# Performance work log

Measured on AMD Instinct MI355X. Metric: run time of the kernel, lower is better.

## Reference

```python
import jax, jax.numpy as jnp
import numpy as np

B, H, N, D, T = 4, 16, 1024, 64, 4

def setup_inputs() -> dict:
    key = jax.random.key(0)
    kq, kk, kv, ka, kw = jax.random.split(key, 5)
    Q = jax.random.normal(kq, (B, H, N, D), dtype=jnp.float32)
    K = jax.random.normal(kk, (B, H, N, D), dtype=jnp.float32)
    V = jax.random.normal(kv, (B, H, N, D), dtype=jnp.float32)
    # stacked adjacency matrices, one [B, N, N] per edge type
    A = jax.random.uniform(ka, (T, B, N, N), dtype=jnp.float32)
    # per-edge-type, per-head learned scalar bias weights (glorot-init scalars in torch)
    weight_E = jax.random.normal(kw, (T, H), dtype=jnp.float32)
    return {"Q": Q, "K": K, "V": V, "A": A, "weight_E": weight_E}

def reference(Q, K, V, A, weight_E):
    scale = Q.shape[-1] ** 0.5
    # raw scores [B, H, N, N]
    attn_score = jnp.einsum("bhnd,bhmd->bhnm", Q, K)
    # B_E = sum_t attn_score * (A_t * w_t)  ->  attn_score * sum_t (A_t * w_t)
    bias_factor = jnp.einsum("tbnm,th->bhnm", A, weight_E)
    attn_score = (attn_score + attn_score * bias_factor) / scale
    attn_weight = jax.nn.softmax(attn_score, axis=-1)
    out = jnp.einsum("bhnm,bhmd->bhnd", attn_weight, V)  # dropout p=0.0 is identity
    return out, attn_weight
```

## Files before the change

kernel.cpp:

```cpp
#include <hip/hip_runtime.h>


#define NB 4
#define NH 16
#define NN 1024
#define ND 64
#define NT 4

typedef short s16x4 __attribute__((ext_vector_type(4)));
typedef short s16x8 __attribute__((ext_vector_type(8)));
typedef float f32x4 __attribute__((ext_vector_type(4)));

__device__ __forceinline__ short f2bf(float f) {
  return __builtin_bit_cast(short, (__bf16)f);
}
__device__ __forceinline__ float bf2f(short s) {
  return __builtin_bit_cast(float, ((unsigned)(unsigned short)s) << 16);
}

__device__ __forceinline__ void gload_lds16(const void* g, void* l) {
  __builtin_amdgcn_global_load_lds(
      (const __attribute__((address_space(1))) unsigned int*)g,
      (__attribute__((address_space(3))) unsigned int*)l, 16, 0, 0);
}

__global__ void pack_k(const float* __restrict__ Kg, short* __restrict__ Khi,
                       short* __restrict__ Klo) {
  int t = blockIdx.x * 256 + threadIdx.x;
  int p0 = t * 8;
  int bh = p0 >> 16;
  int rem = p0 & 65535;
  int chunk = rem >> 12;
  int e = rem & 4095;
  int r = e >> 6;
  int dd0 = e & 63;
  int d0 = dd0 ^ ((r & 7) << 3);
  const float* src = Kg + ((size_t)bh * NN + chunk * 64 + r) * ND + d0;
  float4 a = *reinterpret_cast<const float4*>(src);
  float4 c4 = *reinterpret_cast<const float4*>(src + 4);
  float f[8] = {a.x, a.y, a.z, a.w, c4.x, c4.y, c4.z, c4.w};
  s16x8 hi, lo;
#pragma unroll
  for (int j = 0; j < 8; ++j) {
    short h = f2bf(f[j]);
    hi[j] = h;
    lo[j] = f2bf(f[j] - bf2f(h));
  }
  *reinterpret_cast<s16x8*>(Khi + p0) = hi;
  *reinterpret_cast<s16x8*>(Klo + p0) = lo;
}

__global__ void pack_vt(const float* __restrict__ Vg, short* __restrict__ Vt) {
  __shared__ float tile[64 * 65];
  int bh = blockIdx.x >> 4;
  int kc = blockIdx.x & 15;
  int tid = threadIdx.x;
#pragma unroll
  for (int i = 0; i < 4; ++i) {
    int e = tid + i * 256;
    int k = e >> 4, d0 = (e & 15) * 4;
    const float* src = Vg + ((size_t)bh * NN + kc * 64 + k) * ND + d0;
    float4 v = *reinterpret_cast<const float4*>(src);
    float* dst = &tile[k * 65 + d0];
    dst[0] = v.x; dst[1] = v.y; dst[2] = v.z; dst[3] = v.w;
  }
  __syncthreads();
  {
    int d = tid >> 2;
    int kk = (tid & 3) * 16;
    s16x8 o0, o1;
#pragma unroll
    for (int j = 0; j < 8; ++j) o0[j] = f2bf(tile[(kk + j) * 65 + d]);
#pragma unroll
    for (int j = 0; j < 8; ++j) o1[j] = f2bf(tile[(kk + 8 + j) * 65 + d]);
    short* dst = Vt + ((size_t)bh * ND + d) * NN + kc * 64 + kk;
    *reinterpret_cast<s16x8*>(dst) = o0;
    *reinterpret_cast<s16x8*>(dst + 8) = o1;
  }
}

__global__ __launch_bounds__(256, 3) void mrsa_main(
    const float* __restrict__ Qg, const float* __restrict__ Ag,
    const float* __restrict__ Wg, const short* __restrict__ Khi,
    const short* __restrict__ Klo, const short* __restrict__ Vt,
    float* __restrict__ outO, float* __restrict__ outW) {
  __shared__ short smem[16384];
  __shared__ float red0[16][4];
  __shared__ float red1[16][4];

  const int tid = threadIdx.x;
  const int lane = tid & 63;
  const int wv = tid >> 6;
  const int l4 = lane & 15;
  const int hi4 = lane >> 4;

  const int x = blockIdx.x & 7;
  const int i = blockIdx.x >> 3;
  const int b = x >> 1;
  const int h = ((i >> 5) & 1) * 8 + (i & 7);
  const int rb = (x & 1) * 32 + ((i >> 6) << 2) + ((i >> 3) & 3);
  const int row0 = rb * 16;

  const size_t bh = (size_t)b * NH + h;
  const float* Qp = Qg + bh * (NN * ND);

  float wE[NT];
#pragma unroll
  for (int t = 0; t < NT; ++t) wE[t] = Wg[t * NH + h];

  const int k0 = hi4 * 8;

  s16x8 qh[2], ql[2];
#pragma unroll
  for (int ks = 0; ks < 2; ++ks) {
    const float* qrow = Qp + (size_t)(row0 + l4) * ND + ks * 32 + k0;
#pragma unroll
    for (int j = 0; j < 8; ++j) {
      float f = qrow[j];
      short hb = f2bf(f);
      qh[ks][j] = hb;
      ql[ks][j] = f2bf(f - bf2f(hb));
    }
  }

  const int bcol = wv * 16 + l4;
  const int bsw = (bcol & 7) << 3;
  const size_t kbase = bh * 65536;

  const float* Ap[NT];
#pragma unroll
  for (int t = 0; t < NT; ++t)
    Ap[t] = Ag + ((size_t)t * NB + b) * (NN * NN) +
            (size_t)(row0 + hi4 * 4) * NN + bcol;

  f32x4 sAcc[16];
  float aBuf[2][NT][4];

#define STAGE_K(cc)                                                         \
  do {                                                                      \
    size_t g0 =                                                             \
        kbase + (size_t)(cc)*4096 + (size_t)wv * 1024 + (size_t)lane * 8;   \
    short* KH = &smem[((cc)&1) * 8192];                                     \
    short* KL = KH + 4096;                                                  \
    gload_lds16(Khi + g0, KH + wv * 1024);                                  \
    gload_lds16(Khi + g0 + 512, KH + wv * 1024 + 512);                      \
    gload_lds16(Klo + g0, KL + wv * 1024);                                  \
    gload_lds16(Klo + g0 + 512, KL + wv * 1024 + 512);                      \
  } while (0)

#define ISSUE_A(cc)                                                         \
  do {                                                                      \
    _Pragma("unroll") for (int t = 0; t < NT; ++t) {                        \
      _Pragma("unroll") for (int r = 0; r < 4; ++r) {                       \
        aBuf[(cc)&1][t][r] = Ap[t][r * NN + (cc)*64];                       \
      }                                                                     \
    }                                                                       \
  } while (0)

  STAGE_K(0);
  ISSUE_A(0);

#pragma unroll
  for (int c = 0; c < 16; ++c) {
    __syncthreads();
    if (c < 15) {
      STAGE_K(c + 1);
      ISSUE_A(c + 1);
    }
    const short* KH = &smem[(c & 1) * 8192];
    const short* KL = KH + 4096;
    s16x8 kh8[2], kl8[2];
#pragma unroll
    for (int ks = 0; ks < 2; ++ks) {
      int ph = bcol * 64 + ((ks * 32 + k0) ^ bsw);
      kh8[ks] = *reinterpret_cast<const s16x8*>(&KH[ph]);
      kl8[ks] = *reinterpret_cast<const s16x8*>(&KL[ph]);
    }
    f32x4 acc = {0.f, 0.f, 0.f, 0.f};
#pragma unroll
    for (int ks = 0; ks < 2; ++ks) {
      acc = __builtin_amdgcn_mfma_f32_16x16x32_bf16(qh[ks], kh8[ks], acc, 0, 0, 0);
      acc = __builtin_amdgcn_mfma_f32_16x16x32_bf16(qh[ks], kl8[ks], acc, 0, 0, 0);
      acc = __builtin_amdgcn_mfma_f32_16x16x32_bf16(ql[ks], kh8[ks], acc, 0, 0, 0);
    }
#pragma unroll
    for (int r = 0; r < 4; ++r) {
      float bias = wE[0] * aBuf[c & 1][0][r] + wE[1] * aBuf[c & 1][1][r] +
                   wE[2] * aBuf[c & 1][2][r] + wE[3] * aBuf[c & 1][3][r];
      sAcc[c][r] = acc[r] * (1.f + bias) * 0.125f;
    }
  }

  float mr[4];
#pragma unroll
  for (int r = 0; r < 4; ++r) {
    float m = sAcc[0][r];
#pragma unroll
    for (int c = 1; c < 16; ++c) m = fmaxf(m, sAcc[c][r]);
    mr[r] = m;
  }
#pragma unroll
  for (int off = 8; off >= 1; off >>= 1) {
#pragma unroll
    for (int r = 0; r < 4; ++r) mr[r] = fmaxf(mr[r], __shfl_xor(mr[r], off));
  }
  if (l4 == 0) {
#pragma unroll
    for (int r = 0; r < 4; ++r) red0[hi4 * 4 + r][wv] = mr[r];
  }
  __syncthreads();
  float mfin[4], inv[4];
#pragma unroll
  for (int r = 0; r < 4; ++r) {
    float4 v = *reinterpret_cast<const float4*>(&red0[hi4 * 4 + r][0]);
    mfin[r] = fmaxf(fmaxf(v.x, v.y), fmaxf(v.z, v.w));
  }
  float sr[4];
#pragma unroll
  for (int r = 0; r < 4; ++r) {
    float s = 0.f;
#pragma unroll
    for (int c = 0; c < 16; ++c) {
      float e = __expf(sAcc[c][r] - mfin[r]);
      sAcc[c][r] = e;
      s += e;
    }
    sr[r] = s;
  }
#pragma unroll
  for (int off = 8; off >= 1; off >>= 1) {
#pragma unroll
    for (int r = 0; r < 4; ++r) sr[r] += __shfl_xor(sr[r], off);
  }
  if (l4 == 0) {
#pragma unroll
    for (int r = 0; r < 4; ++r) red1[hi4 * 4 + r][wv] = sr[r];
  }
  __syncthreads();
#pragma unroll
  for (int r = 0; r < 4; ++r) {
    float4 v = *reinterpret_cast<const float4*>(&red1[hi4 * 4 + r][0]);
    inv[r] = 1.f / (v.x + v.y + v.z + v.w);
  }

#pragma unroll
  for (int r = 0; r < 4; ++r) {
    const int lrow = hi4 * 4 + r;
    float* gw = outW + ((bh * NN + (size_t)(row0 + lrow)) << 10) + bcol;
    const int prow = lrow * 1024;
    const int swc = bcol ^ ((lrow & 7) << 3);
#pragma unroll
    for (int c = 0; c < 16; ++c) {
      float w = sAcc[c][r] * inv[r];
      __builtin_nontemporal_store(w, &gw[c * 64]);
      smem[prow + c * 64 + swc] = f2bf(w);
    }
  }
  __syncthreads();

  {
    f32x4 acc = {0.f, 0.f, 0.f, 0.f};
    const int dcol = bcol;
    const int abase = l4 * 1024;
    const int asw = (l4 & 7) << 3;
    const short* vtp = Vt + (bh * ND + (size_t)dcol) * NN;
#pragma unroll 8
    for (int kk = 0; kk < 32; ++kk) {
      int kb = kk * 32 + k0;
      s16x8 af = *reinterpret_cast<const s16x8*>(&smem[abase + (kb ^ asw)]);
      s16x8 bfv = *reinterpret_cast<const s16x8*>(&vtp[kb]);
      acc = __builtin_amdgcn_mfma_f32_16x16x32_bf16(af, bfv, acc, 0, 0, 0);
    }
#pragma unroll
    for (int r = 0; r < 4; ++r) {
      __builtin_nontemporal_store(
          acc[r], &outO[(bh * NN + (size_t)(row0 + hi4 * 4 + r)) * ND + dcol]);
    }
  }
#undef STAGE_K
#undef ISSUE_A
}

__global__ __launch_bounds__(256, 2) void mrsa_fused(
    const float* __restrict__ Qg, const float* __restrict__ Kg,
    const float* __restrict__ Vg, const float* __restrict__ Ag,
    const float* __restrict__ Wg, float* __restrict__ outO,
    float* __restrict__ outW) {
  __shared__ short KsHi[64 * 64];
  __shared__ short KsLo[64 * 64];
  __shared__ float Ss[16 * 1024];
  const int tid = threadIdx.x;
  const int lane = tid & 63;
  const int wv = tid >> 6;
  const int rb = blockIdx.x;
  const int h = blockIdx.y;
  const int b = blockIdx.z;
  const int row0 = rb * 16;
  const size_t bh = (size_t)b * NH + h;
  const float* Qp = Qg + bh * (NN * ND);
  const float* Kp = Kg + bh * (NN * ND);
  const float* Vp = Vg + bh * (NN * ND);
  float wE[NT];
#pragma unroll
  for (int t = 0; t < NT; ++t) wE[t] = Wg[t * NH + h];
  const int arow = lane & 15;
  const int k0 = (lane >> 4) * 8;
  s16x8 qh[2], ql[2];
#pragma unroll
  for (int ks = 0; ks < 2; ++ks) {
    const float* qrow = Qp + (size_t)(row0 + arow) * ND + ks * 32 + k0;
#pragma unroll
    for (int j = 0; j < 8; ++j) {
      float f = qrow[j];
      short hi = f2bf(f);
      qh[ks][j] = hi;
      ql[ks][j] = f2bf(f - bf2f(hi));
    }
  }
  const int bcol = wv * 16 + (lane & 15);
  const int bsw = (bcol & 7) << 3;
  for (int c = 0; c < 16; ++c) {
#pragma unroll
    for (int i = 0; i < 4; ++i) {
      int e4 = tid + i * 256;
      int r = e4 >> 4;
      int d0 = (e4 & 15) * 4;
      float4 kv = *reinterpret_cast<const float4*>(
          Kp + (size_t)(c * 64 + r) * ND + d0);
      float kf[4];
      kf[0] = kv.x; kf[1] = kv.y; kf[2] = kv.z; kf[3] = kv.w;
      s16x4 hi4, lo4;
#pragma unroll
      for (int j = 0; j < 4; ++j) {
        short hi = f2bf(kf[j]);
        hi4[j] = hi;
        lo4[j] = f2bf(kf[j] - bf2f(hi));
      }
      int sw = r * 64 + (d0 ^ ((r & 7) << 3));
      *reinterpret_cast<s16x4*>(&KsHi[sw]) = hi4;
      *reinterpret_cast<s16x4*>(&KsLo[sw]) = lo4;
    }
    __syncthreads();
    f32x4 acc = {0.f, 0.f, 0.f, 0.f};
#pragma unroll
    for (int ks = 0; ks < 2; ++ks) {
      int kb = ks * 32 + k0;
      int ph = bcol * 64 + (kb ^ bsw);
      s16x8 kh8 = *reinterpret_cast<const s16x8*>(&KsHi[ph]);
      s16x8 kl8 = *reinterpret_cast<const s16x8*>(&KsLo[ph]);
      acc = __builtin_amdgcn_mfma_f32_16x16x32_bf16(qh[ks], kh8, acc, 0, 0, 0);
      acc = __builtin_amdgcn_mfma_f32_16x16x32_bf16(qh[ks], kl8, acc, 0, 0, 0);
      acc = __builtin_amdgcn_mfma_f32_16x16x32_bf16(ql[ks], kh8, acc, 0, 0, 0);
    }
    int gcol = c * 64 + bcol;
#pragma unroll
    for (int r = 0; r < 4; ++r) {
      int lrow = (lane >> 4) * 4 + r;
      int grow = row0 + lrow;
      float bias = 0.f;
#pragma unroll
      for (int t = 0; t < NT; ++t)
        bias += wE[t] *
                Ag[((size_t)t * NB + b) * (NN * NN) + (size_t)grow * NN + gcol];
      Ss[lrow * 1024 + (gcol ^ ((lrow & 7) << 3))] =
          acc[r] * (1.f + bias) * 0.125f;
    }
    __syncthreads();
  }
#pragma unroll
  for (int rr = 0; rr < 4; ++rr) {
    int lrow = wv * 4 + rr;
    float* srow = &Ss[lrow * 1024];
    int sw = (lrow & 7) << 3;
    float m = -3.4e38f;
#pragma unroll
    for (int i = 0; i < 16; ++i) m = fmaxf(m, srow[i * 64 + lane]);
#pragma unroll
    for (int off = 32; off; off >>= 1) m = fmaxf(m, __shfl_xor(m, off));
    float ev[16];
    float lsum = 0.f;
#pragma unroll
    for (int i = 0; i < 16; ++i) {
      float e = __expf(srow[i * 64 + lane] - m);
      ev[i] = e;
      lsum += e;
    }
#pragma unroll
    for (int off = 32; off; off >>= 1) lsum += __shfl_xor(lsum, off);
    float inv = 1.f / lsum;
    float* gw = outW + (bh * NN + (size_t)(row0 + lrow)) * NN;
#pragma unroll
    for (int i = 0; i < 16; ++i) {
      float w = ev[i] * inv;
      int p = i * 64 + lane;
      srow[p] = w;
      gw[p ^ sw] = w;
    }
  }
  __syncthreads();
  {
    f32x4 acc = {0.f, 0.f, 0.f, 0.f};
    const int dcol = wv * 16 + (lane & 15);
    const int asw = (arow & 7) << 3;
    const float* srow = &Ss[arow * 1024];
#pragma unroll 2
    for (int kk = 0; kk < 32; ++kk) {
      int kb = kk * 32 + k0;
      int ph = kb ^ asw;
      float4 a0 = *reinterpret_cast<const float4*>(&srow[ph]);
      float4 a1 = *reinterpret_cast<const float4*>(&srow[ph + 4]);
      s16x8 af, bfv;
      af[0] = f2bf(a0.x); af[1] = f2bf(a0.y);
      af[2] = f2bf(a0.z); af[3] = f2bf(a0.w);
      af[4] = f2bf(a1.x); af[5] = f2bf(a1.y);
      af[6] = f2bf(a1.z); af[7] = f2bf(a1.w);
      const float* vcol = Vp + (size_t)kb * ND + dcol;
#pragma unroll
      for (int j = 0; j < 8; ++j) bfv[j] = f2bf(vcol[j * ND]);
      acc = __builtin_amdgcn_mfma_f32_16x16x32_bf16(af, bfv, acc, 0, 0, 0);
    }
#pragma unroll
    for (int r = 0; r < 4; ++r) {
      int lrow = (lane >> 4) * 4 + r;
      outO[(bh * NN + (size_t)(row0 + lrow)) * ND + dcol] = acc[r];
    }
  }
}

extern "C" void kernel_launch(void* const* d_in, const int* in_sizes, int n_in,
                              void* d_out, int out_size, void* d_ws,
                              size_t ws_size, hipStream_t stream) {
  const float* Q = (const float*)d_in[0];
  const float* K = (const float*)d_in[1];
  const float* V = (const float*)d_in[2];
  const float* A = (const float*)d_in[3];
  const float* wE = (const float*)d_in[4];
  float* out = (float*)d_out;
  float* outW = out + (size_t)NB * NH * NN * ND;

  const size_t nElem = (size_t)NB * NH * NN * ND;
  const size_t need = 3 * nElem * sizeof(short);
  if (ws_size >= need) {
    short* Khi = (short*)d_ws;
    short* Klo = Khi + nElem;
    short* Vt = Klo + nElem;
    hipLaunchKernelGGL(pack_k, dim3(2048), dim3(256), 0, stream, K, Khi, Klo);
    hipLaunchKernelGGL(pack_vt, dim3(NB * NH * 16), dim3(256), 0, stream, V,
                       Vt);
    hipLaunchKernelGGL(mrsa_main, dim3(4096), dim3(256), 0, stream, Q, A, wE,
                       Khi, Klo, Vt, out, outW);
  } else {
    dim3 grid(NN / 16, NH, NB);
    hipLaunchKernelGGL(mrsa_fused, grid, dim3(256), 0, stream, Q, K, V, A, wE,
                       out, outW);
  }
}
```

Measured before the change: 193.5 us.

## Load adjacency tiles as coalesced float4 and stage bias through LDS

Adjacency values were loaded as scalar per-lane gathers in the MFMA output layout. Now each thread reads float4 rows of A for all four edge types, forms the weighted bias sum, and writes it to a double-buffered, swizzled LDS tile. Each lane then reads its bias back in the accumulator layout. This targets the dominant A bandwidth cost with wider, coalesced loads, at the price of extra LDS traffic, about 8KB more shared memory per block, and a store placed after the compute in each iteration.

```diff
diff --git a/kernel.cpp b/kernel.cpp
--- a/kernel.cpp
+++ b/kernel.cpp
@@ -84,7 +84,8 @@
     const float* __restrict__ Wg, const short* __restrict__ Khi,
     const short* __restrict__ Klo, const short* __restrict__ Vt,
     float* __restrict__ outO, float* __restrict__ outW) {
-  __shared__ short smem[16384];
+  __shared__ short kbuf[16384];
+  __shared__ float abuf[2][1024];
   __shared__ float red0[16][4];
   __shared__ float red1[16][4];
 
@@ -127,20 +128,23 @@
   const int bsw = (bcol & 7) << 3;
   const size_t kbase = bh * 65536;
 
-  const float* Ap[NT];
+  const int arow_w = tid >> 4;
+  const int acol_w = (tid & 15) * 4;
+  const float* Ap2[NT];
 #pragma unroll
   for (int t = 0; t < NT; ++t)
-    Ap[t] = Ag + ((size_t)t * NB + b) * (NN * NN) +
-            (size_t)(row0 + hi4 * 4) * NN + bcol;
+    Ap2[t] = Ag + ((size_t)t * NB + b) * (NN * NN) +
+             (size_t)(row0 + arow_w) * NN + acol_w;
+  const int awsw = acol_w ^ (wv << 3);
 
   f32x4 sAcc[16];
-  float aBuf[2][NT][4];
+  float4 aR[NT];
 
 #define STAGE_K(cc)                                                         \
   do {                                                                      \
     size_t g0 =                                                             \
         kbase + (size_t)(cc)*4096 + (size_t)wv * 1024 + (size_t)lane * 8;   \
-    short* KH = &smem[((cc)&1) * 8192];                                     \
+    short* KH = &kbuf[((cc)&1) * 8192];                                     \
     short* KL = KH + 4096;                                                  \
     gload_lds16(Khi + g0, KH + wv * 1024);                                  \
     gload_lds16(Khi + g0 + 512, KH + wv * 1024 + 512);                      \
@@ -148,26 +152,39 @@
     gload_lds16(Klo + g0 + 512, KL + wv * 1024 + 512);                      \
   } while (0)
 
-#define ISSUE_A(cc)                                                         \
+#define ALOAD(cc)                                                           \
   do {                                                                      \
     _Pragma("unroll") for (int t = 0; t < NT; ++t) {                        \
-      _Pragma("unroll") for (int r = 0; r < 4; ++r) {                       \
-        aBuf[(cc)&1][t][r] = Ap[t][r * NN + (cc)*64];                       \
-      }                                                                     \
+      aR[t] = *reinterpret_cast<const float4*>(&Ap2[t][(cc)*64]);           \
     }                                                                       \
   } while (0)
 
+#define AWRITE(cc)                                                          \
+  do {                                                                      \
+    float4 s4;                                                              \
+    s4.x = wE[0] * aR[0].x + wE[1] * aR[1].x + wE[2] * aR[2].x +            \
+           wE[3] * aR[3].x;                                                 \
+    s4.y = wE[0] * aR[0].y + wE[1] * aR[1].y + wE[2] * aR[2].y +            \
+           wE[3] * aR[3].y;                                                 \
+    s4.z = wE[0] * aR[0].z + wE[1] * aR[1].z + wE[2] * aR[2].z +            \
+           wE[3] * aR[3].z;                                                 \
+    s4.w = wE[0] * aR[0].w + wE[1] * aR[1].w + wE[2] * aR[2].w +            \
+           wE[3] * aR[3].w;                                                 \
+    *reinterpret_cast<float4*>(&abuf[(cc)&1][arow_w * 64 + awsw]) = s4;     \
+  } while (0)
+
   STAGE_K(0);
-  ISSUE_A(0);
+  ALOAD(0);
+  AWRITE(0);
 
 #pragma unroll
   for (int c = 0; c < 16; ++c) {
     __syncthreads();
     if (c < 15) {
       STAGE_K(c + 1);
-      ISSUE_A(c + 1);
-    }
-    const short* KH = &smem[(c & 1) * 8192];
+      ALOAD(c + 1);
+    }
+    const short* KH = &kbuf[(c & 1) * 8192];
     const short* KL = KH + 4096;
     s16x8 kh8[2], kl8[2];
 #pragma unroll
@@ -185,10 +202,11 @@
     }
 #pragma unroll
     for (int r = 0; r < 4; ++r) {
-      float bias = wE[0] * aBuf[c & 1][0][r] + wE[1] * aBuf[c & 1][1][r] +
-                   wE[2] * aBuf[c & 1][2][r] + wE[3] * aBuf[c & 1][3][r];
+      const int row = hi4 * 4 + r;
+      float bias = abuf[c & 1][row * 64 + (bcol ^ (hi4 << 3))];
       sAcc[c][r] = acc[r] * (1.f + bias) * 0.125f;
     }
+    if (c < 15) AWRITE(c + 1);
   }
 
   float mr[4];
@@ -253,7 +271,7 @@
     for (int c = 0; c < 16; ++c) {
       float w = sAcc[c][r] * inv[r];
       __builtin_nontemporal_store(w, &gw[c * 64]);
-      smem[prow + c * 64 + swc] = f2bf(w);
+      kbuf[prow + c * 64 + swc] = f2bf(w);
     }
   }
   __syncthreads();
@@ -267,7 +285,7 @@
 #pragma unroll 8
     for (int kk = 0; kk < 32; ++kk) {
       int kb = kk * 32 + k0;
-      s16x8 af = *reinterpret_cast<const s16x8*>(&smem[abase + (kb ^ asw)]);
+      s16x8 af = *reinterpret_cast<const s16x8*>(&kbuf[abase + (kb ^ asw)]);
       s16x8 bfv = *reinterpret_cast<const s16x8*>(&vtp[kb]);
       acc = __builtin_amdgcn_mfma_f32_16x16x32_bf16(af, bfv, acc, 0, 0, 0);
     }
@@ -278,7 +296,8 @@
     }
   }
 #undef STAGE_K
-#undef ISSUE_A
+#undef ALOAD
+#undef AWRITE
 }
 
 __global__ __launch_bounds__(256, 2) void mrsa_fused(
```

Result: slower. 245.4 us (+26.8%).

## Load packed K fragments directly from global instead of LDS double-buffering

Applied to the files above, without the earlier changes.

Removes the LDS double-buffered staging of K hi/lo chunks (global_load_lds plus a per-chunk __syncthreads) and has each lane read its K fragments straight from global memory. The pack_k kernel now writes K in plain row-major order without the XOR swizzle. The adjacency loads are also no longer prefetched one chunk ahead but issued inside the same iteration, relying on the fully unrolled loop and the compiler to hide latency. This drops barriers and LDS traffic but gives up explicit prefetching and may raise VGPR pressure.

```diff
diff --git a/kernel.cpp b/kernel.cpp
--- a/kernel.cpp
+++ b/kernel.cpp
@@ -18,24 +18,11 @@
   return __builtin_bit_cast(float, ((unsigned)(unsigned short)s) << 16);
 }
 
-__device__ __forceinline__ void gload_lds16(const void* g, void* l) {
-  __builtin_amdgcn_global_load_lds(
-      (const __attribute__((address_space(1))) unsigned int*)g,
-      (__attribute__((address_space(3))) unsigned int*)l, 16, 0, 0);
-}
-
 __global__ void pack_k(const float* __restrict__ Kg, short* __restrict__ Khi,
                        short* __restrict__ Klo) {
   int t = blockIdx.x * 256 + threadIdx.x;
   int p0 = t * 8;
-  int bh = p0 >> 16;
-  int rem = p0 & 65535;
-  int chunk = rem >> 12;
-  int e = rem & 4095;
-  int r = e >> 6;
-  int dd0 = e & 63;
-  int d0 = dd0 ^ ((r & 7) << 3);
-  const float* src = Kg + ((size_t)bh * NN + chunk * 64 + r) * ND + d0;
+  const float* src = Kg + p0;
   float4 a = *reinterpret_cast<const float4*>(src);
   float4 c4 = *reinterpret_cast<const float4*>(src + 4);
   float f[8] = {a.x, a.y, a.z, a.w, c4.x, c4.y, c4.z, c4.w};
@@ -84,7 +71,7 @@
     const float* __restrict__ Wg, const short* __restrict__ Khi,
     const short* __restrict__ Klo, const short* __restrict__ Vt,
     float* __restrict__ outO, float* __restrict__ outW) {
-  __shared__ short smem[16384];
+  __shared__ short pbuf[16384];
   __shared__ float red0[16][4];
   __shared__ float red1[16][4];
 
@@ -124,8 +111,8 @@
   }
 
   const int bcol = wv * 16 + l4;
-  const int bsw = (bcol & 7) << 3;
-  const size_t kbase = bh * 65536;
+  const short* kph = Khi + bh * 65536 + (size_t)bcol * 64 + k0;
+  const short* kpl = Klo + bh * 65536 + (size_t)bcol * 64 + k0;
 
   const float* Ap[NT];
 #pragma unroll
@@ -134,47 +121,20 @@
             (size_t)(row0 + hi4 * 4) * NN + bcol;
 
   f32x4 sAcc[16];
-  float aBuf[2][NT][4];
-
-#define STAGE_K(cc)                                                         \
-  do {                                                                      \
-    size_t g0 =                                                             \
-        kbase + (size_t)(cc)*4096 + (size_t)wv * 1024 + (size_t)lane * 8;   \
-    short* KH = &smem[((cc)&1) * 8192];                                     \
-    short* KL = KH + 4096;                                                  \
-    gload_lds16(Khi + g0, KH + wv * 1024);                                  \
-    gload_lds16(Khi + g0 + 512, KH + wv * 1024 + 512);                      \
-    gload_lds16(Klo + g0, KL + wv * 1024);                                  \
-    gload_lds16(Klo + g0 + 512, KL + wv * 1024 + 512);                      \
-  } while (0)
-
-#define ISSUE_A(cc)                                                         \
-  do {                                                                      \
-    _Pragma("unroll") for (int t = 0; t < NT; ++t) {                        \
-      _Pragma("unroll") for (int r = 0; r < 4; ++r) {                       \
-        aBuf[(cc)&1][t][r] = Ap[t][r * NN + (cc)*64];                       \
-      }                                                                     \
-    }                                                                       \
-  } while (0)
-
-  STAGE_K(0);
-  ISSUE_A(0);
 
 #pragma unroll
   for (int c = 0; c < 16; ++c) {
-    __syncthreads();
-    if (c < 15) {
-      STAGE_K(c + 1);
-      ISSUE_A(c + 1);
-    }
-    const short* KH = &smem[(c & 1) * 8192];
-    const short* KL = KH + 4096;
     s16x8 kh8[2], kl8[2];
 #pragma unroll
     for (int ks = 0; ks < 2; ++ks) {
-      int ph = bcol * 64 + ((ks * 32 + k0) ^ bsw);
-      kh8[ks] = *reinterpret_cast<const s16x8*>(&KH[ph]);
-      kl8[ks] = *reinterpret_cast<const s16x8*>(&KL[ph]);
+      kh8[ks] = *reinterpret_cast<const s16x8*>(kph + c * 4096 + ks * 32);
+      kl8[ks] = *reinterpret_cast<const s16x8*>(kpl + c * 4096 + ks * 32);
+    }
+    float aB[NT][4];
+#pragma unroll
+    for (int t = 0; t < NT; ++t) {
+#pragma unroll
+      for (int r = 0; r < 4; ++r) aB[t][r] = Ap[t][r * NN + c * 64];
     }
     f32x4 acc = {0.f, 0.f, 0.f, 0.f};
 #pragma unroll
@@ -185,8 +145,8 @@
     }
 #pragma unroll
     for (int r = 0; r < 4; ++r) {
-      float bias = wE[0] * aBuf[c & 1][0][r] + wE[1] * aBuf[c & 1][1][r] +
-                   wE[2] * aBuf[c & 1][2][r] + wE[3] * aBuf[c & 1][3][r];
+      float bias = wE[0] * aB[0][r] + wE[1] * aB[1][r] + wE[2] * aB[2][r] +
+                   wE[3] * aB[3][r];
       sAcc[c][r] = acc[r] * (1.f + bias) * 0.125f;
     }
   }
@@ -253,7 +213,7 @@
     for (int c = 0; c < 16; ++c) {
       float w = sAcc[c][r] * inv[r];
       __builtin_nontemporal_store(w, &gw[c * 64]);
-      smem[prow + c * 64 + swc] = f2bf(w);
+      pbuf[prow + c * 64 + swc] = f2bf(w);
     }
   }
   __syncthreads();
@@ -267,7 +227,7 @@
 #pragma unroll 8
     for (int kk = 0; kk < 32; ++kk) {
       int kb = kk * 32 + k0;
-      s16x8 af = *reinterpret_cast<const s16x8*>(&smem[abase + (kb ^ asw)]);
+      s16x8 af = *reinterpret_cast<const s16x8*>(&pbuf[abase + (kb ^ asw)]);
       s16x8 bfv = *reinterpret_cast<const s16x8*>(&vtp[kb]);
       acc = __builtin_amdgcn_mfma_f32_16x16x32_bf16(af, bfv, acc, 0, 0, 0);
     }
@@ -277,8 +237,6 @@
           acc[r], &outO[(bh * NN + (size_t)(row0 + hi4 * 4 + r)) * ND + dcol]);
     }
   }
-#undef STAGE_K
-#undef ISSUE_A
 }
 
 __global__ __launch_bounds__(256, 2) void mrsa_fused(
```

Result: slower. 248.6 us (+28.5%).

## Process 32 rows per 512-thread block and coalesce attention-weight stores via LDS

Applied to the files above, without the earlier changes.

Each block now runs 8 waves covering 32 query rows in two halves that share one staged K tile in LDS. This halves K staging traffic per row and doubles LDS to 64KB per block. The attention-weight output is no longer written as scattered per-lane scalars. It is read back from the bf16 probability tile in LDS and written as contiguous float4 nontemporal stores, so the stored weights now carry bf16 rounding instead of full fp32 precision. The grid shrinks to 2048 blocks of 512 threads with launch bounds adjusted to match.

```diff
diff --git a/kernel.cpp b/kernel.cpp
--- a/kernel.cpp
+++ b/kernel.cpp
@@ -79,27 +79,29 @@
   }
 }
 
-__global__ __launch_bounds__(256, 3) void mrsa_main(
+__global__ __launch_bounds__(512, 2) void mrsa_main(
     const float* __restrict__ Qg, const float* __restrict__ Ag,
     const float* __restrict__ Wg, const short* __restrict__ Khi,
     const short* __restrict__ Klo, const short* __restrict__ Vt,
     float* __restrict__ outO, float* __restrict__ outW) {
-  __shared__ short smem[16384];
-  __shared__ float red0[16][4];
-  __shared__ float red1[16][4];
+  __shared__ short smem[32768];
+  __shared__ float red0[32][4];
+  __shared__ float red1[32][4];
 
   const int tid = threadIdx.x;
   const int lane = tid & 63;
   const int wv = tid >> 6;
   const int l4 = lane & 15;
   const int hi4 = lane >> 4;
+  const int half = wv >> 2;
+  const int wq = wv & 3;
 
   const int x = blockIdx.x & 7;
   const int i = blockIdx.x >> 3;
   const int b = x >> 1;
   const int h = ((i >> 5) & 1) * 8 + (i & 7);
-  const int rb = (x & 1) * 32 + ((i >> 6) << 2) + ((i >> 3) & 3);
-  const int row0 = rb * 16;
+  const int rb = (x & 1) * 16 + ((i >> 6) & 3) * 4 + ((i >> 3) & 3);
+  const int row0 = rb * 32;
 
   const size_t bh = (size_t)b * NH + h;
   const float* Qp = Qg + bh * (NN * ND);
@@ -113,7 +115,8 @@
   s16x8 qh[2], ql[2];
 #pragma unroll
   for (int ks = 0; ks < 2; ++ks) {
-    const float* qrow = Qp + (size_t)(row0 + l4) * ND + ks * 32 + k0;
+    const float* qrow =
+        Qp + (size_t)(row0 + half * 16 + l4) * ND + ks * 32 + k0;
 #pragma unroll
     for (int j = 0; j < 8; ++j) {
       float f = qrow[j];
@@ -123,7 +126,7 @@
     }
   }
 
-  const int bcol = wv * 16 + l4;
+  const int bcol = wq * 16 + l4;
   const int bsw = (bcol & 7) << 3;
   const size_t kbase = bh * 65536;
 
@@ -131,7 +134,7 @@
 #pragma unroll
   for (int t = 0; t < NT; ++t)
     Ap[t] = Ag + ((size_t)t * NB + b) * (NN * NN) +
-            (size_t)(row0 + hi4 * 4) * NN + bcol;
+            (size_t)(row0 + half * 16 + hi4 * 4) * NN + bcol;
 
   f32x4 sAcc[16];
   float aBuf[2][NT][4];
@@ -139,13 +142,11 @@
 #define STAGE_K(cc)                                                         \
   do {                                                                      \
     size_t g0 =                                                             \
-        kbase + (size_t)(cc)*4096 + (size_t)wv * 1024 + (size_t)lane * 8;   \
+        kbase + (size_t)(cc)*4096 + (size_t)wv * 512 + (size_t)lane * 8;    \
     short* KH = &smem[((cc)&1) * 8192];                                     \
     short* KL = KH + 4096;                                                  \
-    gload_lds16(Khi + g0, KH + wv * 1024);                                  \
-    gload_lds16(Khi + g0 + 512, KH + wv * 1024 + 512);                      \
-    gload_lds16(Klo + g0, KL + wv * 1024);                                  \
-    gload_lds16(Klo + g0 + 512, KL + wv * 1024 + 512);                      \
+    gload_lds16(Khi + g0, KH + wv * 512);                                   \
+    gload_lds16(Klo + g0, KL + wv * 512);                                   \
   } while (0)
 
 #define ISSUE_A(cc)                                                         \
@@ -206,13 +207,14 @@
   }
   if (l4 == 0) {
 #pragma unroll
-    for (int r = 0; r < 4; ++r) red0[hi4 * 4 + r][wv] = mr[r];
+    for (int r = 0; r < 4; ++r) red0[half * 16 + hi4 * 4 + r][wq] = mr[r];
   }
   __syncthreads();
   float mfin[4], inv[4];
 #pragma unroll
   for (int r = 0; r < 4; ++r) {
-    float4 v = *reinterpret_cast<const float4*>(&red0[hi4 * 4 + r][0]);
+    float4 v =
+        *reinterpret_cast<const float4*>(&red0[half * 16 + hi4 * 4 + r][0]);
     mfin[r] = fmaxf(fmaxf(v.x, v.y), fmaxf(v.z, v.w));
   }
   float sr[4];
@@ -234,26 +236,24 @@
   }
   if (l4 == 0) {
 #pragma unroll
-    for (int r = 0; r < 4; ++r) red1[hi4 * 4 + r][wv] = sr[r];
+    for (int r = 0; r < 4; ++r) red1[half * 16 + hi4 * 4 + r][wq] = sr[r];
   }
   __syncthreads();
 #pragma unroll
   for (int r = 0; r < 4; ++r) {
-    float4 v = *reinterpret_cast<const float4*>(&red1[hi4 * 4 + r][0]);
+    float4 v =
+        *reinterpret_cast<const float4*>(&red1[half * 16 + hi4 * 4 + r][0]);
     inv[r] = 1.f / (v.x + v.y + v.z + v.w);
   }
 
 #pragma unroll
   for (int r = 0; r < 4; ++r) {
-    const int lrow = hi4 * 4 + r;
-    float* gw = outW + ((bh * NN + (size_t)(row0 + lrow)) << 10) + bcol;
-    const int prow = lrow * 1024;
-    const int swc = bcol ^ ((lrow & 7) << 3);
+    const int row = half * 16 + hi4 * 4 + r;
+    const int prow = row * 1024;
+    const int swc = bcol ^ ((row & 7) << 3);
 #pragma unroll
     for (int c = 0; c < 16; ++c) {
-      float w = sAcc[c][r] * inv[r];
-      __builtin_nontemporal_store(w, &gw[c * 64]);
-      smem[prow + c * 64 + swc] = f2bf(w);
+      smem[prow + c * 64 + swc] = f2bf(sAcc[c][r] * inv[r]);
     }
   }
   __syncthreads();
@@ -261,7 +261,7 @@
   {
     f32x4 acc = {0.f, 0.f, 0.f, 0.f};
     const int dcol = bcol;
-    const int abase = l4 * 1024;
+    const int abase = (half * 16 + l4) * 1024;
     const int asw = (l4 & 7) << 3;
     const short* vtp = Vt + (bh * ND + (size_t)dcol) * NN;
 #pragma unroll 8
@@ -274,7 +274,28 @@
 #pragma unroll
     for (int r = 0; r < 4; ++r) {
       __builtin_nontemporal_store(
-          acc[r], &outO[(bh * NN + (size_t)(row0 + hi4 * 4 + r)) * ND + dcol]);
+          acc[r],
+          &outO[(bh * NN + (size_t)(row0 + half * 16 + hi4 * 4 + r)) * ND +
+                dcol]);
+    }
+  }
+
+#pragma unroll
+  for (int rr = 0; rr < 4; ++rr) {
+    const int row = wv * 4 + rr;
+    const int sw8 = (row & 7) << 3;
+    float* gw = outW + ((bh * NN + (size_t)(row0 + row)) << 10);
+    const int prow = row * 1024;
+#pragma unroll
+    for (int i2 = 0; i2 < 4; ++i2) {
+      int gcol = lane * 4 + i2 * 256;
+      s16x4 p4 = *reinterpret_cast<const s16x4*>(&smem[prow + (gcol ^ sw8)]);
+      f32x4 w4;
+      w4[0] = bf2f(p4[0]);
+      w4[1] = bf2f(p4[1]);
+      w4[2] = bf2f(p4[2]);
+      w4[3] = bf2f(p4[3]);
+      __builtin_nontemporal_store(w4, reinterpret_cast<f32x4*>(&gw[gcol]));
     }
   }
 #undef STAGE_K
@@ -439,15 +460,15 @@
   float* outW = out + (size_t)NB * NH * NN * ND;
 
   const size_t nElem = (size_t)NB * NH * NN * ND;
-  const size_t need = 3 * nElem * sizeof(short);
-  if (ws_size >= need) {
+  const size_t needK = 3 * nElem * sizeof(short);
+  if (ws_size >= needK) {
     short* Khi = (short*)d_ws;
     short* Klo = Khi + nElem;
     short* Vt = Klo + nElem;
     hipLaunchKernelGGL(pack_k, dim3(2048), dim3(256), 0, stream, K, Khi, Klo);
     hipLaunchKernelGGL(pack_vt, dim3(NB * NH * 16), dim3(256), 0, stream, V,
                        Vt);
-    hipLaunchKernelGGL(mrsa_main, dim3(4096), dim3(256), 0, stream, Q, A, wE,
+    hipLaunchKernelGGL(mrsa_main, dim3(2048), dim3(512), 0, stream, Q, A, wE,
                        Khi, Klo, Vt, out, outW);
   } else {
     dim3 grid(NN / 16, NH, NB);
```

Result: slower. 239.3 us (+23.7%).
